# Kernel optimization log

Measured on AMD Instinct MI355X. Metric: run time of the kernel, lower is better.

Reference implementation:

```python
import jax, jax.numpy as jnp
import numpy as np

N = 4
TMAX = 20
EPS = 1e-06
POST_MULT = 2.0


def setup_inputs() -> dict:
    key = jax.random.key(0)
    ks = jax.random.split(key, 8)
    T, C = 8192, 1024
    return {
        "x": jax.random.normal(ks[0], (T, N, C), dtype=jnp.float32),
        "f_out": jax.random.normal(ks[1], (T, C), dtype=jnp.float32),
        "mix": jax.random.normal(ks[2], (T, 2 * N + N * N), dtype=jnp.float32),
        "invr": jax.random.uniform(ks[3], (T,), dtype=jnp.float32),
        "alpha_pre": jax.random.uniform(ks[4], (1,), dtype=jnp.float32),
        "alpha_post": jax.random.uniform(ks[5], (1,), dtype=jnp.float32),
        "alpha_res": jax.random.uniform(ks[6], (1,), dtype=jnp.float32),
        "bias": jax.random.normal(ks[7], (2 * N + N * N,), dtype=jnp.float32),
    }


def _sinkhorn(r):
    # r: (T, N, N) logits. Row-softmax exp, then TMAX row/col normalizations.
    r = jnp.exp(r - jnp.max(r, axis=-1, keepdims=True))
    def body(_, r):
        r = r / (jnp.sum(r, axis=-1, keepdims=True) + EPS)  # row normalize
        r = r / (jnp.sum(r, axis=-2, keepdims=True) + EPS)  # col normalize
        return r
    return jax.lax.fori_loop(0, TMAX, body, r)


def reference(x, f_out, mix, invr, alpha_pre, alpha_post, alpha_res, bias):
    T = mix.shape[0]
    s = mix * invr[:, None]  # (T, 24)
    h_pre = jax.nn.sigmoid(s[:, :N] * alpha_pre + bias[:N])                      # (T, N)
    h_post = jax.nn.sigmoid(s[:, N:2 * N] * alpha_post + bias[N:2 * N]) * POST_MULT  # (T, N)
    r = (s[:, 2 * N:] * alpha_res + bias[2 * N:]).reshape(T, N, N)
    h_res = _sinkhorn(r)  # (T, N, N), doubly-normalized mixing matrix
    # pre-aggregate the N residual streams into one (input to the wrapped sublayer)
    y_pre = jnp.einsum("tn,tnc->tc", h_pre, x)
    # residual remix + gated sublayer output broadcast back to N streams
    out = jnp.einsum("tji,tic->tjc", h_res, x) + h_post[:, :, None] * f_out[:, None, :]
    return y_pre, out
```

## Files before the change

kernel.cpp:

```cpp
#include <hip/hip_runtime.h>
#include <math.h>

#define NN 4
#define TMAX 20
#define EPS 1e-6f
#define POST_MULT 2.0f

typedef float vfloat4 __attribute__((ext_vector_type(4)));

__global__ __launch_bounds__(256) void coeff_kernel(
    const float* __restrict__ mix,
    const float* __restrict__ invr,
    const float* __restrict__ alpha_pre,
    const float* __restrict__ alpha_post,
    const float* __restrict__ alpha_res,
    const float* __restrict__ bias,
    float* __restrict__ coeffs,
    int T)
{
    const int gtid = blockIdx.x * blockDim.x + threadIdx.x;
    const int t    = gtid >> 4;
    const int lane = gtid & 15;
    if (t >= T) return;

    const float ir = invr[t];

    float r = mix[t * 24 + 8 + lane] * ir * alpha_res[0] + bias[8 + lane];
    float m = r;
    m = fmaxf(m, __shfl_xor(m, 1));
    m = fmaxf(m, __shfl_xor(m, 2));
    r = __expf(r - m);
    #pragma unroll
    for (int it = 0; it < TMAX; ++it) {
        float rs = r;
        rs += __shfl_xor(rs, 1);
        rs += __shfl_xor(rs, 2);
        r = r / (rs + EPS);
        float cs = r;
        cs += __shfl_xor(cs, 4);
        cs += __shfl_xor(cs, 8);
        r = r / (cs + EPS);
    }
    coeffs[t * 24 + 8 + lane] = r;

    if (lane < 8) {
        const float a = (lane < NN) ? alpha_pre[0] : alpha_post[0];
        const float z = mix[t * 24 + lane] * ir * a + bias[lane];
        float sg = 1.0f / (1.0f + __expf(-z));
        if (lane >= NN) sg *= POST_MULT;
        coeffs[t * 24 + lane] = sg;
    }
}

__device__ __forceinline__ void process_item(
    long i, int sh, int NV,
    const float* __restrict__ x, const float* __restrict__ f_out,
    const float* __restrict__ coeffs,
    float* __restrict__ y_pre, float* __restrict__ out)
{
    const int t = (int)(i >> sh);
    const int v = (int)(i & (NV - 1));

    const int ts = __builtin_amdgcn_readfirstlane(t);
    const float* cf = coeffs + (size_t)ts * 24;

    const vfloat4* xv4 = (const vfloat4*)x + (size_t)t * NN * NV;
    const vfloat4* fv4 = (const vfloat4*)f_out + (size_t)t * NV;
    vfloat4* yp4 = (vfloat4*)y_pre + (size_t)t * NV;
    vfloat4* o4  = (vfloat4*)out + (size_t)t * NN * NV;

    vfloat4 xv[NN];
    #pragma unroll
    for (int n = 0; n < NN; ++n) xv[n] = xv4[n * NV + v];
    const vfloat4 fv = fv4[v];

    vfloat4 yv = cf[0] * xv[0] + cf[1] * xv[1] + cf[2] * xv[2] + cf[3] * xv[3];
    __builtin_nontemporal_store(yv, &yp4[v]);

    #pragma unroll
    for (int j = 0; j < NN; ++j) {
        vfloat4 ov = cf[4 + j] * fv;
        #pragma unroll
        for (int ii = 0; ii < NN; ++ii) ov += cf[8 + j * 4 + ii] * xv[ii];
        __builtin_nontemporal_store(ov, &o4[j * NV + v]);
    }
}

__global__ __launch_bounds__(256) void stream_kernel(
    const float* __restrict__ x,
    const float* __restrict__ f_out,
    const float* __restrict__ coeffs,
    float* __restrict__ y_pre,
    float* __restrict__ out,
    int C, int T)
{
    const int NV = C >> 2;
    const int sh = 31 - __clz(NV);
    const long M = (long)T << sh;
    const long half = M >> 1;
    const long stride = (long)gridDim.x * blockDim.x;
    const long gid = (long)blockIdx.x * blockDim.x + threadIdx.x;

    for (long i = gid; i < half; i += stride) {
        process_item(i,        sh, NV, x, f_out, coeffs, y_pre, out);
        process_item(i + half, sh, NV, x, f_out, coeffs, y_pre, out);
    }
    for (long i = (half << 1) + gid; i < M; i += stride)
        process_item(i, sh, NV, x, f_out, coeffs, y_pre, out);
}

__global__ __launch_bounds__(256) void stream_fallback(
    const float* __restrict__ x, const float* __restrict__ f_out,
    const float* __restrict__ coeffs,
    float* __restrict__ y_pre, float* __restrict__ out, int C)
{
    const int t   = blockIdx.x;
    const int tid = threadIdx.x;
    const float* cf = coeffs + (size_t)t * 24;

    const int NV = C >> 2;
    const vfloat4* xv4 = (const vfloat4*)(x + (size_t)t * NN * C);
    const vfloat4* fv4 = (const vfloat4*)(f_out + (size_t)t * C);
    vfloat4* yp4 = (vfloat4*)(y_pre + (size_t)t * C);
    vfloat4* o4  = (vfloat4*)(out + (size_t)t * NN * C);

    for (int v = tid; v < NV; v += blockDim.x) {
        vfloat4 xv[NN];
        #pragma unroll
        for (int n = 0; n < NN; ++n) xv[n] = xv4[n * NV + v];
        const vfloat4 fv = fv4[v];

        vfloat4 yv = cf[0] * xv[0] + cf[1] * xv[1] + cf[2] * xv[2] + cf[3] * xv[3];
        __builtin_nontemporal_store(yv, &yp4[v]);

        #pragma unroll
        for (int j = 0; j < NN; ++j) {
            vfloat4 ov = cf[4 + j] * fv;
            #pragma unroll
            for (int i = 0; i < NN; ++i) ov += cf[8 + j * 4 + i] * xv[i];
            __builtin_nontemporal_store(ov, &o4[j * NV + v]);
        }
    }
}

extern "C" void kernel_launch(void* const* d_in, const int* in_sizes, int n_in,
                              void* d_out, int out_size, void* d_ws, size_t ws_size,
                              hipStream_t stream) {
    const float* x          = (const float*)d_in[0];
    const float* f_out      = (const float*)d_in[1];
    const float* mix        = (const float*)d_in[2];
    const float* invr       = (const float*)d_in[3];
    const float* alpha_pre  = (const float*)d_in[4];
    const float* alpha_post = (const float*)d_in[5];
    const float* alpha_res  = (const float*)d_in[6];
    const float* bias       = (const float*)d_in[7];

    const int T = in_sizes[3];
    const int C = in_sizes[1] / T;

    float* y_pre = (float*)d_out;
    float* out   = (float*)d_out + (size_t)T * C;
    float* coeffs = (float*)d_ws;

    const int grid1 = (T * 16 + 255) / 256;
    coeff_kernel<<<grid1, 256, 0, stream>>>(mix, invr, alpha_pre, alpha_post,
                                            alpha_res, bias, coeffs, T);

    const int NV = C >> 2;
    const bool fast = NV > 0 && (NV & (NV - 1)) == 0 && (NV % 64) == 0
                      && (T % 2) == 0;
    if (fast) {
        stream_kernel<<<2048, 256, 0, stream>>>(x, f_out, coeffs, y_pre, out,
                                                C, T);
    } else {
        stream_fallback<<<T, 256, 0, stream>>>(x, f_out, coeffs, y_pre, out, C);
    }
}
```

Before: 302.6 us.

## Add C=1024 specialized kernel batching four tokens per block with loads issued upfront

Replaces the grid-stride persistent stream kernel with a kernel specialized for C=1024 where each 256-thread block handles four tokens and issues all twenty vector loads before any compute or store. This aims to raise memory-level parallelism and remove index arithmetic and loop overhead in the bandwidth-bound streaming pass. The fallback is merged into a single grid-stride kernel for other shapes. Register pressure rises with 20 live vfloat4 values per thread, which may reduce occupancy.

```diff
diff --git a/kernel.cpp b/kernel.cpp
--- a/kernel.cpp
+++ b/kernel.cpp
@@ -52,6 +52,49 @@
     }
 }
 
+#define NVC 256
+
+__global__ __launch_bounds__(256) void stream4_kernel(
+    const float* __restrict__ x,
+    const float* __restrict__ f_out,
+    const float* __restrict__ coeffs,
+    float* __restrict__ y_pre,
+    float* __restrict__ out)
+{
+    const int t0 = blockIdx.x << 2;
+    const int v  = threadIdx.x;
+
+    vfloat4 xd[4][NN];
+    vfloat4 fd[4];
+    #pragma unroll
+    for (int k = 0; k < 4; ++k) {
+        const vfloat4* xp = (const vfloat4*)x + (size_t)(t0 + k) * NN * NVC;
+        #pragma unroll
+        for (int n = 0; n < NN; ++n) xd[k][n] = xp[n * NVC + v];
+        fd[k] = ((const vfloat4*)f_out)[(size_t)(t0 + k) * NVC + v];
+    }
+
+    #pragma unroll
+    for (int k = 0; k < 4; ++k) {
+        const float* cf = coeffs + (size_t)(t0 + k) * 24;
+
+        vfloat4* yp4 = (vfloat4*)y_pre + (size_t)(t0 + k) * NVC;
+        vfloat4* o4  = (vfloat4*)out + (size_t)(t0 + k) * NN * NVC;
+
+        vfloat4 yv = cf[0] * xd[k][0] + cf[1] * xd[k][1]
+                   + cf[2] * xd[k][2] + cf[3] * xd[k][3];
+        __builtin_nontemporal_store(yv, &yp4[v]);
+
+        #pragma unroll
+        for (int j = 0; j < NN; ++j) {
+            vfloat4 ov = cf[4 + j] * fd[k];
+            #pragma unroll
+            for (int i = 0; i < NN; ++i) ov += cf[8 + j * 4 + i] * xd[k][i];
+            __builtin_nontemporal_store(ov, &o4[j * NVC + v]);
+        }
+    }
+}
+
 __device__ __forceinline__ void process_item(
     long i, int sh, int NV,
     const float* __restrict__ x, const float* __restrict__ f_out,
@@ -86,59 +129,42 @@
     }
 }
 
-__global__ __launch_bounds__(256) void stream_kernel(
-    const float* __restrict__ x,
-    const float* __restrict__ f_out,
-    const float* __restrict__ coeffs,
-    float* __restrict__ y_pre,
-    float* __restrict__ out,
-    int C, int T)
-{
-    const int NV = C >> 2;
-    const int sh = 31 - __clz(NV);
-    const long M = (long)T << sh;
-    const long half = M >> 1;
-    const long stride = (long)gridDim.x * blockDim.x;
-    const long gid = (long)blockIdx.x * blockDim.x + threadIdx.x;
-
-    for (long i = gid; i < half; i += stride) {
-        process_item(i,        sh, NV, x, f_out, coeffs, y_pre, out);
-        process_item(i + half, sh, NV, x, f_out, coeffs, y_pre, out);
-    }
-    for (long i = (half << 1) + gid; i < M; i += stride)
-        process_item(i, sh, NV, x, f_out, coeffs, y_pre, out);
-}
-
 __global__ __launch_bounds__(256) void stream_fallback(
     const float* __restrict__ x, const float* __restrict__ f_out,
     const float* __restrict__ coeffs,
-    float* __restrict__ y_pre, float* __restrict__ out, int C)
-{
-    const int t   = blockIdx.x;
-    const int tid = threadIdx.x;
-    const float* cf = coeffs + (size_t)t * 24;
-
+    float* __restrict__ y_pre, float* __restrict__ out, int C, int T)
+{
     const int NV = C >> 2;
-    const vfloat4* xv4 = (const vfloat4*)(x + (size_t)t * NN * C);
-    const vfloat4* fv4 = (const vfloat4*)(f_out + (size_t)t * C);
-    vfloat4* yp4 = (vfloat4*)(y_pre + (size_t)t * C);
-    vfloat4* o4  = (vfloat4*)(out + (size_t)t * NN * C);
-
-    for (int v = tid; v < NV; v += blockDim.x) {
-        vfloat4 xv[NN];
-        #pragma unroll
-        for (int n = 0; n < NN; ++n) xv[n] = xv4[n * NV + v];
-        const vfloat4 fv = fv4[v];
-
-        vfloat4 yv = cf[0] * xv[0] + cf[1] * xv[1] + cf[2] * xv[2] + cf[3] * xv[3];
-        __builtin_nontemporal_store(yv, &yp4[v]);
-
-        #pragma unroll
-        for (int j = 0; j < NN; ++j) {
-            vfloat4 ov = cf[4 + j] * fv;
+    const bool pow2 = NV > 0 && (NV & (NV - 1)) == 0;
+    if (pow2) {
+        const int sh = 31 - __clz(NV);
+        const long M = (long)T << sh;
+        const long stride = (long)gridDim.x * blockDim.x;
+        for (long i = (long)blockIdx.x * blockDim.x + threadIdx.x; i < M;
+             i += stride)
+            process_item(i, sh, NV, x, f_out, coeffs, y_pre, out);
+    } else {
+        const int t   = blockIdx.x % T;
+        const int tid = threadIdx.x;
+        const float* cf = coeffs + (size_t)t * 24;
+        const vfloat4* xv4 = (const vfloat4*)(x + (size_t)t * NN * C);
+        const vfloat4* fv4 = (const vfloat4*)(f_out + (size_t)t * C);
+        vfloat4* yp4 = (vfloat4*)(y_pre + (size_t)t * C);
+        vfloat4* o4  = (vfloat4*)(out + (size_t)t * NN * C);
+        for (int v = tid; v < NV; v += blockDim.x) {
+            vfloat4 xv[NN];
             #pragma unroll
-            for (int i = 0; i < NN; ++i) ov += cf[8 + j * 4 + i] * xv[i];
-            __builtin_nontemporal_store(ov, &o4[j * NV + v]);
+            for (int n = 0; n < NN; ++n) xv[n] = xv4[n * NV + v];
+            const vfloat4 fv = fv4[v];
+            vfloat4 yv = cf[0]*xv[0] + cf[1]*xv[1] + cf[2]*xv[2] + cf[3]*xv[3];
+            __builtin_nontemporal_store(yv, &yp4[v]);
+            #pragma unroll
+            for (int j = 0; j < NN; ++j) {
+                vfloat4 ov = cf[4 + j] * fv;
+                #pragma unroll
+                for (int i = 0; i < NN; ++i) ov += cf[8 + j*4 + i] * xv[i];
+                __builtin_nontemporal_store(ov, &o4[j * NV + v]);
+            }
         }
     }
 }
@@ -166,13 +192,10 @@
     coeff_kernel<<<grid1, 256, 0, stream>>>(mix, invr, alpha_pre, alpha_post,
                                             alpha_res, bias, coeffs, T);
 
-    const int NV = C >> 2;
-    const bool fast = NV > 0 && (NV & (NV - 1)) == 0 && (NV % 64) == 0
-                      && (T % 2) == 0;
-    if (fast) {
-        stream_kernel<<<2048, 256, 0, stream>>>(x, f_out, coeffs, y_pre, out,
-                                                C, T);
+    if (C == 1024 && (T % 4) == 0) {
+        stream4_kernel<<<T / 4, 256, 0, stream>>>(x, f_out, coeffs, y_pre, out);
     } else {
-        stream_fallback<<<T, 256, 0, stream>>>(x, f_out, coeffs, y_pre, out, C);
-    }
-}
+        stream_fallback<<<2048, 256, 0, stream>>>(x, f_out, coeffs, y_pre, out,
+                                                  C, T);
+    }
+}
```

New measurement: 309.6 us. 2.3% more time.
